# Kernel tuning notes

Hardware: AMD Instinct MI355X
Metric: run time of the kernel (lower is better)

The kernel has to match this reference:

```python
import jax, jax.numpy as jnp
import numpy as np

TEMP_EPS = 1e-6


def setup_inputs() -> dict:
    key = jax.random.key(0)
    k1, k2, k3 = jax.random.split(key, 3)
    B, V = 128, 128256
    logits = jax.random.normal(k1, (B, V), dtype=jnp.float32)
    temperatures = jax.random.uniform(k2, (B,), dtype=jnp.float32)
    u = jax.random.uniform(k3, (B, V), dtype=jnp.float32)
    return {"logits": logits, "temperatures": temperatures, "u": u}


def reference(logits, temperatures, u):
    # Faithful vectorized version of the per-row loop:
    #   nan_to_num -> temperature scale -> softmax -> multinomial sample,
    # expressed as a single Gumbel-max over the batch (equivalent sampling
    # distribution), with greedy argmax where temp <= 1e-6.
    logits = jnp.nan_to_num(logits)                       # [B, V]
    greedy = jnp.argmax(logits, axis=-1)                  # [B]

    safe_temp = jnp.maximum(temperatures, TEMP_EPS)[:, None]  # [B, 1]
    scaled = logits / safe_temp                           # [B, V]

    # Gumbel-max trick: argmax(scaled + g), g ~ Gumbel(0,1), samples
    # exactly from softmax(scaled) == the multinomial in the original.
    uc = jnp.clip(u, 1e-10, 1.0 - 1e-7)
    gumbel = -jnp.log(-jnp.log(uc))                       # [B, V]
    sampled = jnp.argmax(scaled + gumbel, axis=-1)        # [B]

    use_greedy = temperatures <= TEMP_EPS                 # [B] bool
    return jnp.where(use_greedy, greedy, sampled)
```

## Files before the change

### kernel.cpp

```cpp
#include <hip/hip_runtime.h>
#include <cfloat>
#include <cstdint>


#define TEMP_EPS 1e-6f

static constexpr int V       = 128256;
static constexpr int V4      = V / 4;
static constexpr int SEGS    = 32;
static constexpr int SEG_V4  = V4 / SEGS;
static constexpr int TAIL    = SEG_V4 - 3 * 256;

__device__ __forceinline__ unsigned long long pack_key(float v, int idx) {
    unsigned b = __float_as_uint(v);
    unsigned mask = (unsigned)(((int)b >> 31)) | 0x80000000u;
    b ^= mask;
    return ((unsigned long long)b << 32) | (unsigned)(~(unsigned)idx);
}

__device__ __forceinline__ unsigned long long umax64(unsigned long long a,
                                                     unsigned long long b) {
    return a > b ? a : b;
}

__device__ __forceinline__ float neg_log_fast(float c) {
    float t = c - 1.0f;
    float p = -1.0f / 6.0f;
    p = __builtin_fmaf(p, t, 0.2f);
    p = __builtin_fmaf(p, t, -0.25f);
    p = __builtin_fmaf(p, t, 1.0f / 3.0f);
    p = __builtin_fmaf(p, t, -0.5f);
    p = __builtin_fmaf(p, t, 1.0f);
    float wpoly = -t * p;
    float whw = -__logf(c);
    return (c >= 0.90625f) ? wpoly : whw;
}

__global__ __launch_bounds__(256) void sampler_partial_kernel(
    const float* __restrict__ logits,
    const float* __restrict__ temps,
    const float* __restrict__ u,
    unsigned long long* __restrict__ partials) {
    const int row = blockIdx.y;
    const int seg = blockIdx.x;
    const int tid = threadIdx.x;

    const float temp = temps[row];
    const bool greedy = (temp <= TEMP_EPS);
    const float safe_temp = fmaxf(temp, TEMP_EPS);
    const float inv_temp = 1.0f / safe_temp;

    const float4* __restrict__ l4 = (const float4*)(logits + (size_t)row * V);
    const float4* __restrict__ u4 = (const float4*)(u + (size_t)row * V);

    const float UC_LO = 1e-10f;
    const float UC_HI = (float)(1.0 - 1e-7);

    const int base = seg * SEG_V4;

    int idx[4];
    idx[0] = base + tid;
    idx[1] = base + 256 + tid;
    idx[2] = base + 512 + tid;
    idx[3] = (tid < TAIL) ? (base + 768 + tid) : (base + tid);

    unsigned long long key = 0ULL;

    if (greedy) {
        float4 lv[4];
#pragma unroll
        for (int k = 0; k < 4; ++k) lv[k] = l4[idx[k]];
#pragma unroll
        for (int k = 0; k < 4; ++k) {
            const int e = idx[k] * 4;
            float m01 = fmaxf(lv[k].x, lv[k].y);
            float m23 = fmaxf(lv[k].z, lv[k].w);
            float m = fmaxf(m01, m23);
            int ei = (lv[k].x == m) ? e
                   : (lv[k].y == m) ? e + 1
                   : (lv[k].z == m) ? e + 2 : e + 3;
            key = umax64(key, pack_key(m, ei));
        }
    } else {
        float4 lv[4], uv[4];
#pragma unroll
        for (int k = 0; k < 4; ++k) lv[k] = l4[idx[k]];
#pragma unroll
        for (int k = 0; k < 4; ++k) uv[k] = u4[idx[k]];

#pragma unroll
        for (int k = 0; k < 4; ++k) {
            const int e = idx[k] * 4;

            float c0 = fminf(fmaxf(uv[k].x, UC_LO), UC_HI);
            float c1 = fminf(fmaxf(uv[k].y, UC_LO), UC_HI);
            float c2 = fminf(fmaxf(uv[k].z, UC_LO), UC_HI);
            float c3 = fminf(fmaxf(uv[k].w, UC_LO), UC_HI);

            float w0 = neg_log_fast(c0);
            float w1 = neg_log_fast(c1);
            float w2 = neg_log_fast(c2);
            float w3 = neg_log_fast(c3);

            float g0 = -__logf(w0);
            float g1 = -__logf(w1);
            float g2 = -__logf(w2);
            float g3 = -__logf(w3);

            float v0 = __builtin_fmaf(lv[k].x, inv_temp, g0);
            float v1 = __builtin_fmaf(lv[k].y, inv_temp, g1);
            float v2 = __builtin_fmaf(lv[k].z, inv_temp, g2);
            float v3 = __builtin_fmaf(lv[k].w, inv_temp, g3);

            float m01 = fmaxf(v0, v1);
            float m23 = fmaxf(v2, v3);
            float m = fmaxf(m01, m23);
            int ei = (v0 == m) ? e
                   : (v1 == m) ? e + 1
                   : (v2 == m) ? e + 2 : e + 3;
            key = umax64(key, pack_key(m, ei));
        }
    }

    for (int o = 32; o > 0; o >>= 1)
        key = umax64(key, __shfl_down(key, o));

    __shared__ unsigned long long sdata[4];
    if ((tid & 63) == 0) sdata[tid >> 6] = key;
    __syncthreads();

    if (tid == 0) {
        for (int w = 1; w < 4; ++w) key = umax64(key, sdata[w]);
        partials[row * SEGS + seg] = key;
    }
}

__global__ __launch_bounds__(64) void sampler_reduce_kernel(
    const unsigned long long* __restrict__ partials,
    int* __restrict__ out) {
    const int row = blockIdx.x;
    const int t = threadIdx.x;
    unsigned long long key = (t < SEGS) ? partials[row * SEGS + t] : 0ULL;
    for (int o = 32; o > 0; o >>= 1)
        key = umax64(key, __shfl_down(key, o));
    if (t == 0)
        out[row] = (int)(~(unsigned)(key & 0xFFFFFFFFull));
}

extern "C" void kernel_launch(void* const* d_in, const int* in_sizes, int n_in,
                              void* d_out, int out_size, void* d_ws, size_t ws_size,
                              hipStream_t stream) {
    const float* logits = (const float*)d_in[0];
    const float* temps  = (const float*)d_in[1];
    const float* u      = (const float*)d_in[2];
    int* out = (int*)d_out;
    const int B = in_sizes[1];

    unsigned long long* partials = (unsigned long long*)d_ws;

    dim3 grid1(SEGS, B);
    hipLaunchKernelGGL(sampler_partial_kernel, grid1, dim3(256), 0, stream,
                       logits, temps, u, partials);
    hipLaunchKernelGGL(sampler_reduce_kernel, dim3(B), dim3(64), 0, stream,
                       partials, out);
}
```

Before: 145.7 us.

## Fuse cross-segment reduction into partial kernel via last-block atomic counter

Removes the separate reduce kernel. Each block publishes its partial key and bumps a per-row atomic counter, and the last block of each row does the final reduction and writes the output. Per-thread accumulation now uses a float/index compare instead of packing a 64-bit key on every step. A hipMemsetAsync is added to zero the counters each call, so one kernel launch is traded for a memset plus atomics.

```diff
diff --git a/kernel.cpp b/kernel.cpp
--- a/kernel.cpp
+++ b/kernel.cpp
@@ -36,11 +36,13 @@
     return (c >= 0.90625f) ? wpoly : whw;
 }
 
-__global__ __launch_bounds__(256) void sampler_partial_kernel(
+__global__ __launch_bounds__(256) void sampler_fused_kernel(
     const float* __restrict__ logits,
     const float* __restrict__ temps,
     const float* __restrict__ u,
-    unsigned long long* __restrict__ partials) {
+    unsigned long long* __restrict__ partials,
+    unsigned int* __restrict__ counters,
+    int* __restrict__ out) {
     const int row = blockIdx.y;
     const int seg = blockIdx.x;
     const int tid = threadIdx.x;
@@ -64,7 +66,8 @@
     idx[2] = base + 512 + tid;
     idx[3] = (tid < TAIL) ? (base + 768 + tid) : (base + tid);
 
-    unsigned long long key = 0ULL;
+    float best_v = -FLT_MAX;
+    int   best_i = 0x7FFFFFFF;
 
     if (greedy) {
         float4 lv[4];
@@ -79,7 +82,7 @@
             int ei = (lv[k].x == m) ? e
                    : (lv[k].y == m) ? e + 1
                    : (lv[k].z == m) ? e + 2 : e + 3;
-            key = umax64(key, pack_key(m, ei));
+            if (m > best_v) { best_v = m; best_i = ei; }
         }
     } else {
         float4 lv[4], uv[4];
@@ -118,33 +121,41 @@
             int ei = (v0 == m) ? e
                    : (v1 == m) ? e + 1
                    : (v2 == m) ? e + 2 : e + 3;
-            key = umax64(key, pack_key(m, ei));
+            if (m > best_v) { best_v = m; best_i = ei; }
         }
     }
+
+    unsigned long long key = pack_key(best_v, best_i);
 
     for (int o = 32; o > 0; o >>= 1)
         key = umax64(key, __shfl_down(key, o));
 
     __shared__ unsigned long long sdata[4];
+    __shared__ int slast;
     if ((tid & 63) == 0) sdata[tid >> 6] = key;
     __syncthreads();
 
     if (tid == 0) {
         for (int w = 1; w < 4; ++w) key = umax64(key, sdata[w]);
-        partials[row * SEGS + seg] = key;
+        __hip_atomic_store(&partials[row * SEGS + seg], key,
+                           __ATOMIC_RELEASE, __HIP_MEMORY_SCOPE_AGENT);
+        unsigned prev = __hip_atomic_fetch_add(&counters[row], 1u,
+                                               __ATOMIC_ACQ_REL,
+                                               __HIP_MEMORY_SCOPE_AGENT);
+        slast = (prev == SEGS - 1) ? 1 : 0;
     }
-}
+    __syncthreads();
 
-__global__ __launch_bounds__(64) void sampler_reduce_kernel(
-    const unsigned long long* __restrict__ partials,
-    int* __restrict__ out) {
-    const int row = blockIdx.x;
-    const int t = threadIdx.x;
-    unsigned long long key = (t < SEGS) ? partials[row * SEGS + t] : 0ULL;
-    for (int o = 32; o > 0; o >>= 1)
-        key = umax64(key, __shfl_down(key, o));
-    if (t == 0)
-        out[row] = (int)(~(unsigned)(key & 0xFFFFFFFFull));
+    if (slast && tid < 64) {
+        unsigned long long k2 = 0ULL;
+        if (tid < SEGS)
+            k2 = __hip_atomic_load(&partials[row * SEGS + tid],
+                                   __ATOMIC_ACQUIRE, __HIP_MEMORY_SCOPE_AGENT);
+        for (int o = 32; o > 0; o >>= 1)
+            k2 = umax64(k2, __shfl_down(k2, o));
+        if (tid == 0)
+            out[row] = (int)(~(unsigned)(k2 & 0xFFFFFFFFull));
+    }
 }
 
 extern "C" void kernel_launch(void* const* d_in, const int* in_sizes, int n_in,
@@ -157,10 +168,11 @@
     const int B = in_sizes[1];
 
     unsigned long long* partials = (unsigned long long*)d_ws;
+    unsigned int* counters = (unsigned int*)(partials + B * SEGS);
 
-    dim3 grid1(SEGS, B);
-    hipLaunchKernelGGL(sampler_partial_kernel, grid1, dim3(256), 0, stream,
-                       logits, temps, u, partials);
-    hipLaunchKernelGGL(sampler_reduce_kernel, dim3(B), dim3(64), 0, stream,
-                       partials, out);
+    hipMemsetAsync(counters, 0, B * sizeof(unsigned int), stream);
+
+    dim3 grid(SEGS, B);
+    hipLaunchKernelGGL(sampler_fused_kernel, grid, dim3(256), 0, stream,
+                       logits, temps, u, partials, counters, out);
 }
```

Measured after the change: 466.8 us. 3.2x slower.
